# Kernel tuning notes

Measured on AMD Instinct MI355X. Metric: run time of the kernel, lower is better.

## Reference

```python
import jax, jax.numpy as jnp
import numpy as np

E, B, L, H1, H2, C = 8, 4096, 512, 1024, 512, 40


def setup_inputs() -> dict:
    key = jax.random.key(0)
    ks = jax.random.split(key, 9)
    return {
        "x_s": jax.random.normal(ks[0], (B, L), jnp.float32),
        "x_p": jax.random.normal(ks[1], (B, L), jnp.float32),
        "W1": jax.random.normal(ks[2], (E, 2 * L, H1), jnp.float32) / np.sqrt(2 * L).astype(np.float32),
        "b1": jax.random.normal(ks[3], (E, H1), jnp.float32) * 0.01,
        "W2": jax.random.normal(ks[4], (E, H1, H2), jnp.float32) / np.sqrt(H1).astype(np.float32),
        "b2": jax.random.normal(ks[5], (E, H2), jnp.float32) * 0.01,
        "W3": jax.random.normal(ks[6], (E, H2, C), jnp.float32) / np.sqrt(H2).astype(np.float32),
        "b3": jax.random.normal(ks[7], (E, C), jnp.float32) * 0.01,
        "sub_module_label": jax.random.randint(ks[8], (B,), 0, E, dtype=jnp.int32),
        "sub_id": 0,
    }


def reference(x_s, x_p, W1, b1, W2, b2, W3, b3, sub_module_label, sub_id):
    # Encoders (EEGNet/SCN/DCN) abstracted as identity: x_s / x_p are latent features.
    # Cls_HEAD.forward: x = cat([x_p, x_s], dim=1); per-sample routed 3-layer ELU MLP head.
    # Dropout is identity in eval mode.
    x = jnp.concatenate([x_p, x_s], axis=1)                      # [B, 2L]
    h = jax.nn.elu(jnp.einsum('bi,eih->ebh', x, W1) + b1[:, None, :])   # [E, B, H1]
    h = jax.nn.elu(jnp.einsum('ebh,ehk->ebk', h, W2) + b2[:, None, :])  # [E, B, H2]
    out_all = jnp.einsum('ebk,ekc->ebc', h, W3) + b3[:, None, :]        # [E, B, C]
    # select each sample's routed expert output
    bidx = jnp.arange(x.shape[0])
    return out_all[sub_module_label, bidx]                       # [B, C]
```

## Files before the change

kernel.cpp:

```cpp
#include <hip/hip_runtime.h>
#include <hip/hip_bf16.h>
#include <math.h>

#define En   8
#define Bn   4096
#define Ln   512
#define K1n  1024
#define H1n  1024
#define H2n  512
#define Cn   40
#define NP3  48

typedef unsigned short u16;
typedef __attribute__((ext_vector_type(8))) short bf16x8;
typedef __attribute__((ext_vector_type(4))) float f32x4;

__device__ __forceinline__ u16 f2b(float f) {
    union { float f; unsigned int u; } v; v.f = f;
    unsigned int r = v.u + 0x7FFF + ((v.u >> 16) & 1);
    return (u16)(r >> 16);
}

__device__ __forceinline__ void g2l16(const void* g, void* l) {
    __builtin_amdgcn_global_load_lds(
        (const __attribute__((address_space(1))) unsigned int*)(unsigned long long)g,
        (__attribute__((address_space(3))) unsigned int*)(unsigned int)(unsigned long long)l,
        16, 0, 0);
}

__global__ __launch_bounds__(1024) void route_kernel(
    const int* __restrict__ label, int* __restrict__ meta, int* __restrict__ perm)
{
    __shared__ int cnt[En];
    __shared__ int off[En + 1];
    const int tid = threadIdx.x;
    if (tid < En) cnt[tid] = 0;
    __syncthreads();
    for (int b = tid; b < Bn; b += 1024) atomicAdd(&cnt[label[b]], 1);
    __syncthreads();
    if (tid == 0) {
        int run = 0;
        for (int e = 0; e < En; e++) { off[e] = run; run += cnt[e]; }
        off[En] = run;
    }
    __syncthreads();
    if (tid < En) cnt[tid] = off[tid];
    __syncthreads();
    for (int b = tid; b < Bn; b += 1024) {
        int e = label[b];
        int pos = atomicAdd(&cnt[e], 1);
        perm[pos] = b;
    }
    if (tid <= En) meta[tid] = off[tid];
}

__global__ __launch_bounds__(256) void xgather_kernel(
    const float* __restrict__ xp, const float* __restrict__ xs,
    const int* __restrict__ perm, u16* __restrict__ Xb)
{
    const int r = blockIdx.x;
    const int smp = perm[r];
    const int tid = threadIdx.x;
    #pragma unroll
    for (int i = 0; i < 4; i++) {
        int k = tid + i * 256;
        float v = (k < Ln) ? xp[(size_t)smp * Ln + k] : xs[(size_t)smp * Ln + (k - Ln)];
        Xb[(size_t)r * K1n + k] = f2b(v);
    }
}

__global__ __launch_bounds__(256) void wtrans_kernel(
    const float* __restrict__ W, u16* __restrict__ Wt, int K, int N)
{
    __shared__ u16 t[32][33];
    const int tid = threadIdx.x;
    const int k0 = blockIdx.x * 32, n0 = blockIdx.y * 32, e = blockIdx.z;
    const float* Wsrc = W + (size_t)e * K * N;
    u16* Wdst = Wt + (size_t)e * N * K;
    #pragma unroll
    for (int s = 0; s < 4; s++) {
        int kk = (tid >> 5) + s * 8;
        int nn = tid & 31;
        t[kk][nn] = f2b(Wsrc[(size_t)(k0 + kk) * N + n0 + nn]);
    }
    __syncthreads();
    #pragma unroll
    for (int s = 0; s < 4; s++) {
        int nn = (tid >> 5) + s * 8;
        int kk = tid & 31;
        Wdst[(size_t)(n0 + nn) * K + k0 + kk] = t[kk][nn];
    }
}

__global__ __launch_bounds__(256) void w3trans_kernel(
    const float* __restrict__ W3, u16* __restrict__ Wt3)
{
    __shared__ float t[32][41];
    const int e = blockIdx.x, k0 = blockIdx.y * 32;
    const float* src = W3 + (size_t)e * H2n * Cn;
    u16* dst = Wt3 + (size_t)e * NP3 * H2n;
    const int tid = threadIdx.x;
    #pragma unroll
    for (int s = 0; s < 5; s++) {
        int idx = tid + s * 256;
        int kk = idx / Cn, nn = idx - kk * Cn;
        if (kk < 32) t[kk][nn] = src[(size_t)(k0 + kk) * Cn + nn];
    }
    __syncthreads();
    #pragma unroll
    for (int s = 0; s < 6; s++) {
        int idx = tid + s * 256;
        int nn = idx >> 5, kk = idx & 31;
        float v = (nn < Cn) ? t[kk][nn] : 0.f;
        dst[(size_t)nn * H2n + k0 + kk] = f2b(v);
    }
}

template <int K, int N>
__global__ __launch_bounds__(256) void mfma_gemm(
    const u16* __restrict__ A, const u16* __restrict__ Wt,
    const float* __restrict__ bias, const int* __restrict__ meta,
    u16* __restrict__ out)
{
    constexpr int TM = 128, TN = 128, BK = 32;
    __shared__ __align__(16) u16 As[TM * BK];
    __shared__ __align__(16) u16 Bs[TN * BK];
    __shared__ int s_off[En + 1];

    const int tid = threadIdx.x;
    if (tid <= En) s_off[tid] = meta[tid];
    __syncthreads();

    int expert = -1, row0 = 0, acc_t = 0;
    const int bx = blockIdx.x;
    for (int e = 0; e < En; e++) {
        int c = s_off[e + 1] - s_off[e];
        int t = (c + TM - 1) / TM;
        if (expert < 0 && bx < acc_t + t) {
            expert = e;
            row0 = s_off[e] + (bx - acc_t) * TM;
        }
        acc_t += t;
    }
    if (expert < 0) return;
    const int rowmax = s_off[expert + 1] - 1;

    const int col0 = blockIdx.y * TN;
    const u16* Wexp = Wt + (size_t)expert * N * K;

    const int lane = tid & 63;
    const int wid = tid >> 6;
    const int wm = (wid & 1) * 64;
    const int wn = (wid >> 1) * 64;
    const int l15 = lane & 15;
    const int lq = lane >> 4;

    const u16* aptr[2];
    const u16* bptr[2];
    u16* alds[2]; u16* blds[2];
    #pragma unroll
    for (int s = 0; s < 2; s++) {
        int idx = tid + s * 256;
        int rl = idx >> 2, c = idx & 3;
        int kq = c ^ (rl & 3);
        int rg = row0 + rl; if (rg > rowmax) rg = rowmax;
        aptr[s] = A + (size_t)rg * K + kq * 8;
        bptr[s] = Wexp + (size_t)(col0 + rl) * K + kq * 8;
        alds[s] = &As[idx * 8];
        blds[s] = &Bs[idx * 8];
    }

    const int rsw = (0 ^ (l15 & 3));

    f32x4 acc[4][4];
    #pragma unroll
    for (int i = 0; i < 4; i++)
        #pragma unroll
        for (int j = 0; j < 4; j++) acc[i][j] = (f32x4){0.f, 0.f, 0.f, 0.f};

    for (int k0 = 0; k0 < K; k0 += BK) {
        #pragma unroll
        for (int s = 0; s < 2; s++) {
            g2l16(aptr[s] + k0, alds[s]);
            g2l16(bptr[s] + k0, blds[s]);
        }
        __syncthreads();

        const int ksw = (lq ^ rsw) * 8;
        bf16x8 af[4], bf[4];
        #pragma unroll
        for (int i = 0; i < 4; i++)
            af[i] = *(const bf16x8*)&As[(wm + i * 16 + l15) * BK + ksw];
        #pragma unroll
        for (int j = 0; j < 4; j++)
            bf[j] = *(const bf16x8*)&Bs[(wn + j * 16 + l15) * BK + ksw];

        #pragma unroll
        for (int i = 0; i < 4; i++)
            #pragma unroll
            for (int j = 0; j < 4; j++)
                acc[i][j] = __builtin_amdgcn_mfma_f32_16x16x32_bf16(
                    af[i], bf[j], acc[i][j], 0, 0, 0);
        __syncthreads();
    }

    #pragma unroll
    for (int i = 0; i < 4; i++) {
        #pragma unroll
        for (int j = 0; j < 4; j++) {
            int col = col0 + wn + j * 16 + l15;
            float bv = bias[expert * N + col];
            #pragma unroll
            for (int r = 0; r < 4; r++) {
                int grow = row0 + wm + i * 16 + lq * 4 + r;
                if (grow <= rowmax) {
                    float v = acc[i][j][r] + bv;
                    v = (v > 0.f) ? v : (expf(v) - 1.f);
                    out[(size_t)grow * N + col] = f2b(v);
                }
            }
        }
    }
}

__global__ __launch_bounds__(256) void gemm3_mfma(
    const u16* __restrict__ h2, const u16* __restrict__ Wt3,
    const float* __restrict__ b3, const int* __restrict__ meta,
    const int* __restrict__ perm, float* __restrict__ out)
{
    constexpr int TM = 64, BK = 32;
    __shared__ __align__(16) u16 As[TM * BK];
    __shared__ __align__(16) u16 Bs[NP3 * BK];
    __shared__ int s_off[En + 1];

    const int tid = threadIdx.x;
    if (tid <= En) s_off[tid] = meta[tid];
    __syncthreads();

    int expert = -1, row0 = 0, acc_t = 0;
    const int bx = blockIdx.x;
    for (int e = 0; e < En; e++) {
        int c = s_off[e + 1] - s_off[e];
        int t = (c + TM - 1) / TM;
        if (expert < 0 && bx < acc_t + t) {
            expert = e;
            row0 = s_off[e] + (bx - acc_t) * TM;
        }
        acc_t += t;
    }
    if (expert < 0) return;
    const int rowmax = s_off[expert + 1] - 1;

    const int lane = tid & 63;
    const int wid = tid >> 6;
    const int l15 = lane & 15;
    const int lq = lane >> 4;

    const int rl = tid >> 2, c = tid & 3;
    const int kq = c ^ (rl & 3);
    int rg = row0 + rl; if (rg > rowmax) rg = rowmax;
    const u16* ag = h2 + (size_t)rg * H2n + kq * 8;
    const u16* bg = Wt3 + (size_t)expert * NP3 * H2n + (size_t)rl * H2n + kq * 8;
    u16* al = &As[tid * 8];
    u16* bl = &Bs[tid * 8];

    f32x4 acc[3];
    #pragma unroll
    for (int j = 0; j < 3; j++) acc[j] = (f32x4){0.f, 0.f, 0.f, 0.f};

    for (int k0 = 0; k0 < H2n; k0 += BK) {
        g2l16(ag + k0, al);
        if (tid < NP3 * 4) g2l16(bg + k0, bl);
        __syncthreads();

        const int ksw = (lq ^ (l15 & 3)) * 8;
        bf16x8 af = *(const bf16x8*)&As[(wid * 16 + l15) * BK + ksw];
        bf16x8 bf[3];
        #pragma unroll
        for (int j = 0; j < 3; j++)
            bf[j] = *(const bf16x8*)&Bs[(j * 16 + l15) * BK + ksw];
        #pragma unroll
        for (int j = 0; j < 3; j++)
            acc[j] = __builtin_amdgcn_mfma_f32_16x16x32_bf16(af, bf[j], acc[j], 0, 0, 0);
        __syncthreads();
    }

    #pragma unroll
    for (int j = 0; j < 3; j++) {
        int col = j * 16 + l15;
        if (col < Cn) {
            float bv = b3[expert * Cn + col];
            #pragma unroll
            for (int r = 0; r < 4; r++) {
                int grow = row0 + wid * 16 + lq * 4 + r;
                if (grow <= rowmax) {
                    int smp = perm[grow];
                    out[(size_t)smp * Cn + col] = acc[j][r] + bv;
                }
            }
        }
    }
}

extern "C" void kernel_launch(void* const* d_in, const int* in_sizes, int n_in,
                              void* d_out, int out_size, void* d_ws, size_t ws_size,
                              hipStream_t stream)
{
    const float* xs = (const float*)d_in[0];
    const float* xp = (const float*)d_in[1];
    const float* W1 = (const float*)d_in[2];
    const float* b1 = (const float*)d_in[3];
    const float* W2 = (const float*)d_in[4];
    const float* b2 = (const float*)d_in[5];
    const float* W3 = (const float*)d_in[6];
    const float* b3 = (const float*)d_in[7];
    const int* label = (const int*)d_in[8];
    float* out = (float*)d_out;

    char* ws = (char*)d_ws;
    int* meta = (int*)ws;
    int* perm = (int*)(ws + 64);
    u16* Xb  = (u16*)(ws + (64 << 10));
    u16* h2b = Xb;
    u16* W1t = (u16*)(ws + (64 << 10) + (8  << 20));
    u16* W2t = (u16*)(ws + (64 << 10) + (24 << 20));
    u16* h1b = (u16*)(ws + (64 << 10) + (32 << 20));
    u16* W3t = (u16*)(ws + (64 << 10) + (40 << 20));

    route_kernel<<<1, 1024, 0, stream>>>(label, meta, perm);
    xgather_kernel<<<Bn, 256, 0, stream>>>(xp, xs, perm, Xb);
    wtrans_kernel<<<dim3(K1n / 32, H1n / 32, En), 256, 0, stream>>>(W1, W1t, K1n, H1n);
    wtrans_kernel<<<dim3(H1n / 32, H2n / 32, En), 256, 0, stream>>>(W2, W2t, H1n, H2n);
    w3trans_kernel<<<dim3(En, H2n / 32), 256, 0, stream>>>(W3, W3t);

    mfma_gemm<K1n, H1n><<<dim3(40, H1n / 128), 256, 0, stream>>>(Xb, W1t, b1, meta, h1b);
    mfma_gemm<H1n, H2n><<<dim3(40, H2n / 128), 256, 0, stream>>>(h1b, W2t, b2, meta, h2b);

    gemm3_mfma<<<72, 256, 0, stream>>>(h2b, W3t, b3, meta, perm, out);
}
```

Baseline: 199.9 us.

## Fuse routing, input conversion and weight transposes into one prep kernel

```diff
diff --git a/kernel.cpp b/kernel.cpp
--- a/kernel.cpp
+++ b/kernel.cpp
@@ -28,99 +28,120 @@
         16, 0, 0);
 }
 
-__global__ __launch_bounds__(1024) void route_kernel(
-    const int* __restrict__ label, int* __restrict__ meta, int* __restrict__ perm)
-{
-    __shared__ int cnt[En];
-    __shared__ int off[En + 1];
+#define PB_X0   1
+#define PB_X    256
+#define PB_W1   2048
+#define PB_W2   1024
+#define PB_W3   128
+#define PB_TOT  (PB_X0 + PB_X + PB_W1 + PB_W2 + PB_W3)
+
+__device__ __forceinline__ void wtrans64(
+    const float* __restrict__ Wsrc, u16* __restrict__ Wdst,
+    int K, int N, int k0, int n0, int tid, float* sm )
+{
+    #pragma unroll
+    for (int s = 0; s < 4; s++) {
+        int idx = tid + s * 256;
+        int kk = idx >> 4, c4 = (idx & 15) * 4;
+        float4 v = *(const float4*)&Wsrc[(size_t)(k0 + kk) * N + n0 + c4];
+        float* row = sm + kk * 65 + c4;
+        row[0] = v.x; row[1] = v.y; row[2] = v.z; row[3] = v.w;
+    }
+    __syncthreads();
+    #pragma unroll
+    for (int s = 0; s < 4; s++) {
+        int idx = tid + s * 256;
+        int nn = idx >> 4, kc = (idx & 15) * 4;
+        ushort4 o = make_ushort4(f2b(sm[(kc + 0) * 65 + nn]), f2b(sm[(kc + 1) * 65 + nn]),
+                                 f2b(sm[(kc + 2) * 65 + nn]), f2b(sm[(kc + 3) * 65 + nn]));
+        *(ushort4*)&Wdst[(size_t)(n0 + nn) * K + k0 + kc] = o;
+    }
+}
+
+__global__ __launch_bounds__(256) void prep_kernel(
+    const float* __restrict__ xs, const float* __restrict__ xp,
+    const float* __restrict__ W1, const float* __restrict__ W2,
+    const float* __restrict__ W3, const int* __restrict__ label,
+    int* __restrict__ meta, int* __restrict__ perm,
+    u16* __restrict__ Xb, u16* __restrict__ W1t,
+    u16* __restrict__ W2t, u16* __restrict__ W3t)
+{
+    __shared__ __align__(16) float sm[64 * 65];
+    const int bid = blockIdx.x;
     const int tid = threadIdx.x;
-    if (tid < En) cnt[tid] = 0;
-    __syncthreads();
-    for (int b = tid; b < Bn; b += 1024) atomicAdd(&cnt[label[b]], 1);
-    __syncthreads();
-    if (tid == 0) {
-        int run = 0;
-        for (int e = 0; e < En; e++) { off[e] = run; run += cnt[e]; }
-        off[En] = run;
-    }
-    __syncthreads();
-    if (tid < En) cnt[tid] = off[tid];
-    __syncthreads();
-    for (int b = tid; b < Bn; b += 1024) {
-        int e = label[b];
-        int pos = atomicAdd(&cnt[e], 1);
-        perm[pos] = b;
-    }
-    if (tid <= En) meta[tid] = off[tid];
-}
-
-__global__ __launch_bounds__(256) void xgather_kernel(
-    const float* __restrict__ xp, const float* __restrict__ xs,
-    const int* __restrict__ perm, u16* __restrict__ Xb)
-{
-    const int r = blockIdx.x;
-    const int smp = perm[r];
-    const int tid = threadIdx.x;
-    #pragma unroll
-    for (int i = 0; i < 4; i++) {
-        int k = tid + i * 256;
-        float v = (k < Ln) ? xp[(size_t)smp * Ln + k] : xs[(size_t)smp * Ln + (k - Ln)];
-        Xb[(size_t)r * K1n + k] = f2b(v);
-    }
-}
-
-__global__ __launch_bounds__(256) void wtrans_kernel(
-    const float* __restrict__ W, u16* __restrict__ Wt, int K, int N)
-{
-    __shared__ u16 t[32][33];
-    const int tid = threadIdx.x;
-    const int k0 = blockIdx.x * 32, n0 = blockIdx.y * 32, e = blockIdx.z;
-    const float* Wsrc = W + (size_t)e * K * N;
-    u16* Wdst = Wt + (size_t)e * N * K;
-    #pragma unroll
-    for (int s = 0; s < 4; s++) {
-        int kk = (tid >> 5) + s * 8;
-        int nn = tid & 31;
-        t[kk][nn] = f2b(Wsrc[(size_t)(k0 + kk) * N + n0 + nn]);
-    }
-    __syncthreads();
-    #pragma unroll
-    for (int s = 0; s < 4; s++) {
-        int nn = (tid >> 5) + s * 8;
-        int kk = tid & 31;
-        Wdst[(size_t)(n0 + nn) * K + k0 + kk] = t[kk][nn];
-    }
-}
-
-__global__ __launch_bounds__(256) void w3trans_kernel(
-    const float* __restrict__ W3, u16* __restrict__ Wt3)
-{
-    __shared__ float t[32][41];
-    const int e = blockIdx.x, k0 = blockIdx.y * 32;
-    const float* src = W3 + (size_t)e * H2n * Cn;
-    u16* dst = Wt3 + (size_t)e * NP3 * H2n;
-    const int tid = threadIdx.x;
-    #pragma unroll
-    for (int s = 0; s < 5; s++) {
-        int idx = tid + s * 256;
-        int kk = idx / Cn, nn = idx - kk * Cn;
-        if (kk < 32) t[kk][nn] = src[(size_t)(k0 + kk) * Cn + nn];
-    }
-    __syncthreads();
-    #pragma unroll
-    for (int s = 0; s < 6; s++) {
-        int idx = tid + s * 256;
-        int nn = idx >> 5, kk = idx & 31;
-        float v = (nn < Cn) ? t[kk][nn] : 0.f;
-        dst[(size_t)nn * H2n + k0 + kk] = f2b(v);
-    }
-}
-
-template <int K, int N>
+
+    if (bid == 0) {
+        int* cnt = (int*)sm;
+        int* off = cnt + En;
+        if (tid < En) cnt[tid] = 0;
+        __syncthreads();
+        for (int b = tid; b < Bn; b += 256) atomicAdd(&cnt[label[b]], 1);
+        __syncthreads();
+        if (tid == 0) {
+            int run = 0;
+            for (int e = 0; e < En; e++) { off[e] = run; run += cnt[e]; }
+            off[En] = run;
+        }
+        __syncthreads();
+        if (tid < En) cnt[tid] = off[tid];
+        __syncthreads();
+        for (int b = tid; b < Bn; b += 256) {
+            int e = label[b];
+            perm[atomicAdd(&cnt[e], 1)] = b;
+        }
+        if (tid <= En) meta[tid] = off[tid];
+    } else if (bid < PB_X0 + PB_X) {
+        int r0 = (bid - PB_X0) * 16;
+        #pragma unroll 4
+        for (int s = 0; s < 16; s++) {
+            int r = r0 + s;
+            int k = tid * 4;
+            const float* src = (k < Ln) ? (xp + (size_t)r * Ln + k)
+                                        : (xs + (size_t)r * Ln + (k - Ln));
+            float4 v = *(const float4*)src;
+            *(ushort4*)&Xb[(size_t)r * K1n + k] =
+                make_ushort4(f2b(v.x), f2b(v.y), f2b(v.z), f2b(v.w));
+        }
+    } else if (bid < PB_X0 + PB_X + PB_W1) {
+        int b = bid - (PB_X0 + PB_X);
+        int e = b >> 8, rem = b & 255;
+        int k0 = (rem >> 4) * 64, n0 = (rem & 15) * 64;
+        wtrans64(W1 + (size_t)e * K1n * H1n, W1t + (size_t)e * H1n * K1n,
+                 K1n, H1n, k0, n0, tid, sm);
+    } else if (bid < PB_X0 + PB_X + PB_W1 + PB_W2) {
+        int b = bid - (PB_X0 + PB_X + PB_W1);
+        int e = b >> 7, rem = b & 127;
+        int k0 = (rem >> 3) * 64, n0 = (rem & 7) * 64;
+        wtrans64(W2 + (size_t)e * H1n * H2n, W2t + (size_t)e * H2n * H1n,
+                 H1n, H2n, k0, n0, tid, sm);
+    } else {
+        int b = bid - (PB_X0 + PB_X + PB_W1 + PB_W2);
+        int e = b >> 4, k0 = (b & 15) * 32;
+        const float* src = W3 + (size_t)e * H2n * Cn;
+        u16* dst = W3t + (size_t)e * NP3 * H2n;
+        float* t = sm;
+        #pragma unroll
+        for (int s = 0; s < 5; s++) {
+            int idx = tid + s * 256;
+            int kk = idx / Cn, nn = idx - kk * Cn;
+            if (kk < 32) t[kk * 41 + nn] = src[(size_t)(k0 + kk) * Cn + nn];
+        }
+        __syncthreads();
+        #pragma unroll
+        for (int s = 0; s < 6; s++) {
+            int idx = tid + s * 256;
+            int nn = idx >> 5, kk = idx & 31;
+            float v = (nn < Cn) ? t[kk * 41 + nn] : 0.f;
+            dst[(size_t)nn * H2n + k0 + kk] = f2b(v);
+        }
+    }
+}
+
+template <int K, int N, bool GATHER>
 __global__ __launch_bounds__(256) void mfma_gemm(
     const u16* __restrict__ A, const u16* __restrict__ Wt,
     const float* __restrict__ bias, const int* __restrict__ meta,
-    u16* __restrict__ out)
+    const int* __restrict__ perm, u16* __restrict__ out)
 {
     constexpr int TM = 128, TN = 128, BK = 32;
     __shared__ __align__(16) u16 As[TM * BK];
@@ -164,13 +185,14 @@
         int rl = idx >> 2, c = idx & 3;
         int kq = c ^ (rl & 3);
         int rg = row0 + rl; if (rg > rowmax) rg = rowmax;
+        if (GATHER) rg = perm[rg];
         aptr[s] = A + (size_t)rg * K + kq * 8;
         bptr[s] = Wexp + (size_t)(col0 + rl) * K + kq * 8;
         alds[s] = &As[idx * 8];
         blds[s] = &Bs[idx * 8];
     }
 
-    const int rsw = (0 ^ (l15 & 3));
+    const int rsw = l15 & 3;
 
     f32x4 acc[4][4];
     #pragma unroll
@@ -327,14 +349,13 @@
     u16* h1b = (u16*)(ws + (64 << 10) + (32 << 20));
     u16* W3t = (u16*)(ws + (64 << 10) + (40 << 20));
 
-    route_kernel<<<1, 1024, 0, stream>>>(label, meta, perm);
-    xgather_kernel<<<Bn, 256, 0, stream>>>(xp, xs, perm, Xb);
-    wtrans_kernel<<<dim3(K1n / 32, H1n / 32, En), 256, 0, stream>>>(W1, W1t, K1n, H1n);
-    wtrans_kernel<<<dim3(H1n / 32, H2n / 32, En), 256, 0, stream>>>(W2, W2t, H1n, H2n);
-    w3trans_kernel<<<dim3(En, H2n / 32), 256, 0, stream>>>(W3, W3t);
-
-    mfma_gemm<K1n, H1n><<<dim3(40, H1n / 128), 256, 0, stream>>>(Xb, W1t, b1, meta, h1b);
-    mfma_gemm<H1n, H2n><<<dim3(40, H2n / 128), 256, 0, stream>>>(h1b, W2t, b2, meta, h2b);
+    prep_kernel<<<PB_TOT, 256, 0, stream>>>(
+        xs, xp, W1, W2, W3, label, meta, perm, Xb, W1t, W2t, W3t);
+
+    mfma_gemm<K1n, H1n, true><<<dim3(40, H1n / 128), 256, 0, stream>>>(
+        Xb, W1t, b1, meta, perm, h1b);
+    mfma_gemm<H1n, H2n, false><<<dim3(40, H2n / 128), 256, 0, stream>>>(
+        h1b, W2t, b2, meta, perm, h2b);
 
     gemm3_mfma<<<72, 256, 0, stream>>>(h2b, W3t, b3, meta, perm, out);
 }
```

After: 192.8 us. 3.5% less time.
